# Optimization experiments

Measured on AMD Instinct MI355X. Metric: run time of the kernel, lower is better.

The kernel has to match this reference:

```python
import jax, jax.numpy as jnp
import numpy as np

EPS = 1e-5
K = 7        # deformable/spatial kernel size
GRID = 4     # local pool grid size


def conv(x, w, pad=0):
    # x: NCHW, w: OIHW
    return jax.lax.conv_general_dilated(
        x, w, (1, 1), [(pad, pad), (pad, pad)],
        dimension_numbers=('NCHW', 'OIHW', 'NCHW'))


def bn(x, g, b, m, v):
    # eval-mode batchnorm with running stats
    scale = (g * jax.lax.rsqrt(v + EPS))[None, :, None, None]
    return (x - m[None, :, None, None]) * scale + b[None, :, None, None]


def grid_sample(feat, grid):
    # bilinear, padding_mode='zeros', align_corners=False
    # feat: [b,c,h,w], grid: [b,h,w,2] with (x,y) in [-1,1]
    b, c, h, w = feat.shape
    gx = (grid[..., 0] + 1.0) * (w * 0.5) - 0.5
    gy = (grid[..., 1] + 1.0) * (h * 0.5) - 0.5
    x0 = jnp.floor(gx)
    y0 = jnp.floor(gy)
    wx = gx - x0
    wy = gy - y0
    feat_flat = feat.reshape(b, c, h * w)

    def gather(yi, xi):
        valid = (xi >= 0) & (xi < w) & (yi >= 0) & (yi < h)
        xi_c = jnp.clip(xi, 0, w - 1).astype(jnp.int32)
        yi_c = jnp.clip(yi, 0, h - 1).astype(jnp.int32)
        idx = (yi_c * w + xi_c).reshape(b, 1, h * w)
        vals = jnp.take_along_axis(feat_flat, idx, axis=2).reshape(b, c, h, w)
        return vals * valid[:, None].astype(feat.dtype)

    out = (gather(y0, x0) * ((1 - wx) * (1 - wy))[:, None]
           + gather(y0, x0 + 1) * (wx * (1 - wy))[:, None]
           + gather(y0 + 1, x0) * ((1 - wx) * wy)[:, None]
           + gather(y0 + 1, x0 + 1) * (wx * wy)[:, None])
    return out


def cmife_forward(x, align_w, align_g, align_b, align_m, align_v,
                  mlp_w1, mlp_w2, loc_w1, loc_w2, fusion_w,
                  off_w1, off_g, off_bt, off_m, off_v, off_w2, off_b2,
                  attn_w):
    # ---- align: 1x1 conv + BN + SiLU ----
    x = conv(x, align_w)
    x = bn(x, align_g, align_b, align_m, align_v)
    x = x * jax.nn.sigmoid(x)  # SiLU
    b_, c_, h_, w_ = x.shape

    # ---- LocalGlobalChannelAttention ----
    def mlp(z):
        return conv(jax.nn.relu(conv(z, mlp_w1)), mlp_w2)

    g_avg = mlp(jnp.mean(x, (2, 3), keepdims=True))
    g_max = mlp(jnp.max(x, (2, 3), keepdims=True))
    global_attn = g_avg + g_max
    # adaptive avg pool to GRIDxGRID (h,w divisible by GRID)
    loc = x.reshape(b_, c_, GRID, h_ // GRID, GRID, w_ // GRID).mean((3, 5))
    local_attn = conv(jax.nn.relu(conv(loc, loc_w1)), loc_w2)
    local_attn = local_attn.mean((2, 3), keepdims=True)
    alpha = jax.nn.sigmoid(fusion_w)
    ca = jax.nn.sigmoid(alpha * global_attn + (1 - alpha) * local_attn)
    x = ca * x

    # ---- DeformableSpatialAttention ----
    avg_out = jnp.mean(x, 1, keepdims=True)
    max_out = jnp.max(x, 1, keepdims=True)
    sf = jnp.concatenate([avg_out, max_out], axis=1)  # [b,2,h,w]
    o = jax.nn.relu(bn(conv(sf, off_w1, pad=1), off_g, off_bt, off_m, off_v))
    o = conv(o, off_w2, pad=1) + off_b2[None, :, None, None]  # [b,2*K*K,h,w]
    off = o.reshape(b_, 2, K * K, h_, w_).mean(2)             # [b,2,h,w]
    off = jnp.tanh(off) * 0.5
    off = jnp.transpose(off, (0, 2, 3, 1))                    # [b,h,w,2]
    gy, gx = jnp.meshgrid(jnp.linspace(-1.0, 1.0, h_),
                          jnp.linspace(-1.0, 1.0, w_), indexing='ij')
    base = jnp.stack([gx, gy], axis=-1)[None]                 # [1,h,w,2]
    dgrid = jnp.clip(base + off, -1.0, 1.0)
    sampled = grid_sample(sf, dgrid)                          # [b,2,h,w]
    sa = jax.nn.sigmoid(conv(sampled, attn_w, pad=K // 2))    # [b,1,h,w]
    return sa * x


def setup_inputs() -> dict:
    key = jax.random.key(0)
    ks = jax.random.split(key, 24)
    B, CIN, COUT, H, W, MID = 8, 256, 256, 160, 160, 16
    f = jnp.float32
    inp = {
        'x': jax.random.normal(ks[0], (B, CIN, H, W), f),
        'align_w': jax.random.normal(ks[1], (COUT, CIN, 1, 1), f) * 0.05,
        'align_g': jax.random.uniform(ks[2], (COUT,), f, 0.5, 1.5),
        'align_b': jax.random.normal(ks[3], (COUT,), f) * 0.1,
        'align_m': jax.random.normal(ks[4], (COUT,), f) * 0.1,
        'align_v': jax.random.uniform(ks[5], (COUT,), f, 0.5, 1.5),
        'mlp_w1': jax.random.normal(ks[6], (MID, COUT, 1, 1), f) * 0.1,
        'mlp_w2': jax.random.normal(ks[7], (COUT, MID, 1, 1), f) * 0.1,
        'loc_w1': jax.random.normal(ks[8], (MID, COUT, 1, 1), f) * 0.1,
        'loc_w2': jax.random.normal(ks[9], (COUT, MID, 1, 1), f) * 0.1,
        'fusion_w': jnp.float32(0.5),
        'off_w1': jax.random.normal(ks[10], (16, 2, 3, 3), f) * 0.1,
        'off_g': jax.random.uniform(ks[11], (16,), f, 0.5, 1.5),
        'off_bt': jax.random.normal(ks[12], (16,), f) * 0.1,
        'off_m': jax.random.normal(ks[13], (16,), f) * 0.1,
        'off_v': jax.random.uniform(ks[14], (16,), f, 0.5, 1.5),
        'off_w2': jax.random.normal(ks[15], (2 * K * K, 16, 3, 3), f) * 0.01,
        'off_b2': jax.random.normal(ks[16], (2 * K * K,), f) * 0.01,
        'attn_w': jax.random.normal(ks[17], (1, 2, K, K), f) * 0.1,
    }
    return inp


def reference(x, align_w, align_g, align_b, align_m, align_v,
              mlp_w1, mlp_w2, loc_w1, loc_w2, fusion_w,
              off_w1, off_g, off_bt, off_m, off_v, off_w2, off_b2,
              attn_w):
    return cmife_forward(x, align_w, align_g, align_b, align_m, align_v,
                         mlp_w1, mlp_w2, loc_w1, loc_w2, fusion_w,
                         off_w1, off_g, off_bt, off_m, off_v, off_w2, off_b2,
                         attn_w)
```

## Files before the change

### kernel.cpp

```cpp
#include <hip/hip_runtime.h>
#include <hip/hip_bf16.h>

#define HH 160
#define WW 160
#define HW 25600
#define NC 256
#define NB 8

typedef short short8 __attribute__((ext_vector_type(8)));
typedef float f32x4 __attribute__((ext_vector_type(4)));

__device__ __forceinline__ unsigned short f2bf(float f) {
    unsigned u = __float_as_uint(f);
    u += 0x7fffu + ((u >> 16) & 1u);
    return (unsigned short)(u >> 16);
}
__device__ __forceinline__ float bf2f(unsigned short h) {
    return __uint_as_float(((unsigned)h) << 16);
}

__global__ void k0_fold(const float* __restrict__ aw, const float* __restrict__ ag,
                        const float* __restrict__ ab, const float* __restrict__ am,
                        const float* __restrict__ av,
                        unsigned short* __restrict__ wpkh, unsigned short* __restrict__ wpkl,
                        float* __restrict__ biasp) {
    int co = blockIdx.x, t = threadIdx.x;
    float sc = ag[co] * rsqrtf(av[co] + 1e-5f);
    float w = aw[co * 256 + t] * sc;
    unsigned short h = f2bf(w);
    int kk = t >> 5, kq = t & 31;
    wpkh[kk * 10240 + co * 40 + kq] = h;
    wpkl[kk * 10240 + co * 40 + kq] = f2bf(w - bf2f(h));
    if (t == 0) biasp[co] = ab[co] - am[co] * sc;
}

__global__ void k0b_fold2(const float* __restrict__ ow2, const float* __restrict__ ob2,
                          float* __restrict__ weff, float* __restrict__ beff) {
    int t = threadIdx.x;
    if (t < 288) {
        int g = t / 144, r = t - g * 144;
        float s = 0.f;
        for (int q = 0; q < 49; q++) s += ow2[(size_t)(g * 49 + q) * 144 + r];
        weff[t] = s * (1.f / 49.f);
    }
    if (t < 2) {
        float s = 0.f;
        for (int q = 0; q < 49; q++) s += ob2[t * 49 + q];
        beff[t] = s * (1.f / 49.f);
    }
}

__global__ __launch_bounds__(256, 2) void k1_gemm(
    const float* __restrict__ X, const unsigned short* __restrict__ Wph,
    const unsigned short* __restrict__ Wpl,
    const float* __restrict__ biasp, float* __restrict__ xal) {
    __shared__ __align__(16) unsigned short Ah[10240];
    __shared__ __align__(16) unsigned short Al[10240];
    __shared__ __align__(16) unsigned short Bh[5120];
    __shared__ __align__(16) unsigned short Bl[5120];

    int t = threadIdx.x;
    int n0 = blockIdx.x * 128;
    int b  = blockIdx.y;
    const float* Xb = X + (size_t)b * NC * HW;

    int lane = t & 63, wv = t >> 6;
    int lcol = lane & 15, lq = lane >> 4;

    f32x4 acc[4][8];
#pragma unroll
    for (int i = 0; i < 4; i++)
#pragma unroll
        for (int j = 0; j < 8; j++) { f32x4 z = {0.f, 0.f, 0.f, 0.f}; acc[i][j] = z; }

    int bn2 = t & 63;
    int bkq = t >> 6;

    float2 pf[8];

#pragma unroll
    for (int j2 = 0; j2 < 2; j2++) {
        int kq = bkq + 4 * j2;
        const float* src = Xb + (size_t)(kq * 4) * HW + n0 + bn2 * 2;
#pragma unroll
        for (int j = 0; j < 2; j++) {
            pf[j2 * 4 + 2 * j]     = *(const float2*)(src + (size_t)(2 * j) * HW);
            pf[j2 * 4 + 2 * j + 1] = *(const float2*)(src + (size_t)(2 * j + 1) * HW);
        }
    }
    {
        const char* gah = (const char*)Wph;
        const char* gal = (const char*)Wpl;
#pragma unroll
        for (int i = 0; i < 5; i++) {
            int off = wv * 1024 + i * 4096;
            __builtin_amdgcn_global_load_lds(
                (const __attribute__((address_space(1))) unsigned int*)(gah + off + lane * 16),
                (__attribute__((address_space(3))) unsigned int*)((char*)Ah + off),
                16, 0, 0);
            __builtin_amdgcn_global_load_lds(
                (const __attribute__((address_space(1))) unsigned int*)(gal + off + lane * 16),
                (__attribute__((address_space(3))) unsigned int*)((char*)Al + off),
                16, 0, 0);
        }
    }

    for (int kk = 0; kk < 8; kk++) {
#pragma unroll
        for (int j2 = 0; j2 < 2; j2++) {
            int kq = bkq + 4 * j2;
            unsigned h0[2], h1[2], l0[2], l1[2];
#pragma unroll
            for (int j = 0; j < 2; j++) {
                float2 v0 = pf[j2 * 4 + 2 * j];
                float2 v1 = pf[j2 * 4 + 2 * j + 1];
                unsigned short a = f2bf(v0.x), bq = f2bf(v1.x);
                unsigned short c = f2bf(v0.y), d = f2bf(v1.y);
                h0[j] = (unsigned)a | ((unsigned)bq << 16);
                h1[j] = (unsigned)c | ((unsigned)d << 16);
                unsigned short la = f2bf(v0.x - bf2f(a)), lb = f2bf(v1.x - bf2f(bq));
                unsigned short lc = f2bf(v0.y - bf2f(c)), ld = f2bf(v1.y - bf2f(d));
                l0[j] = (unsigned)la | ((unsigned)lb << 16);
                l1[j] = (unsigned)lc | ((unsigned)ld << 16);
            }
            *(uint2*)(&Bh[(bn2 * 2) * 40 + kq * 4])     = make_uint2(h0[0], h0[1]);
            *(uint2*)(&Bh[(bn2 * 2 + 1) * 40 + kq * 4]) = make_uint2(h1[0], h1[1]);
            *(uint2*)(&Bl[(bn2 * 2) * 40 + kq * 4])     = make_uint2(l0[0], l0[1]);
            *(uint2*)(&Bl[(bn2 * 2 + 1) * 40 + kq * 4]) = make_uint2(l1[0], l1[1]);
        }
        __syncthreads();

        short8 afh[4], afl[4];
#pragma unroll
        for (int mt = 0; mt < 4; mt++) {
            afh[mt] = *(const short8*)(&Ah[(wv * 64 + mt * 16 + lcol) * 40 + lq * 8]);
            afl[mt] = *(const short8*)(&Al[(wv * 64 + mt * 16 + lcol) * 40 + lq * 8]);
        }
        if (kk < 7) {
#pragma unroll
            for (int j2 = 0; j2 < 2; j2++) {
                int kq = bkq + 4 * j2;
                const float* src = Xb + (size_t)((kk + 1) * 32 + kq * 4) * HW + n0 + bn2 * 2;
#pragma unroll
                for (int j = 0; j < 2; j++) {
                    pf[j2 * 4 + 2 * j]     = *(const float2*)(src + (size_t)(2 * j) * HW);
                    pf[j2 * 4 + 2 * j + 1] = *(const float2*)(src + (size_t)(2 * j + 1) * HW);
                }
            }
        }
#pragma unroll
        for (int nt = 0; nt < 8; nt++) {
            short8 bh = *(const short8*)(&Bh[(nt * 16 + lcol) * 40 + lq * 8]);
            short8 bl = *(const short8*)(&Bl[(nt * 16 + lcol) * 40 + lq * 8]);
#pragma unroll
            for (int mt = 0; mt < 4; mt++) {
                acc[mt][nt] = __builtin_amdgcn_mfma_f32_16x16x32_bf16(
                    afh[mt], bh, acc[mt][nt], 0, 0, 0);
                acc[mt][nt] = __builtin_amdgcn_mfma_f32_16x16x32_bf16(
                    afh[mt], bl, acc[mt][nt], 0, 0, 0);
                acc[mt][nt] = __builtin_amdgcn_mfma_f32_16x16x32_bf16(
                    afl[mt], bh, acc[mt][nt], 0, 0, 0);
            }
        }
        asm volatile("s_barrier" ::: "memory");
        if (kk < 7) {
            const char* gah = (const char*)(Wph + (kk + 1) * 10240);
            const char* gal = (const char*)(Wpl + (kk + 1) * 10240);
#pragma unroll
            for (int i = 0; i < 5; i++) {
                int off = wv * 1024 + i * 4096;
                __builtin_amdgcn_global_load_lds(
                    (const __attribute__((address_space(1))) unsigned int*)(gah + off + lane * 16),
                    (__attribute__((address_space(3))) unsigned int*)((char*)Ah + off),
                    16, 0, 0);
                __builtin_amdgcn_global_load_lds(
                    (const __attribute__((address_space(1))) unsigned int*)(gal + off + lane * 16),
                    (__attribute__((address_space(3))) unsigned int*)((char*)Al + off),
                    16, 0, 0);
            }
        }
    }
#pragma unroll
    for (int mt = 0; mt < 4; mt++) {
#pragma unroll
        for (int r = 0; r < 4; r++) {
            int co = wv * 64 + mt * 16 + lq * 4 + r;
            float bias = biasp[co];
            size_t rowbase = ((size_t)b * NC + co) * HW + n0;
#pragma unroll
            for (int nt = 0; nt < 8; nt++) {
                int n = nt * 16 + lcol;
                float y = acc[mt][nt][r] + bias;
                float z = y / (1.f + __expf(-y));
                xal[rowbase + n] = z;
            }
        }
    }
}

__global__ void ka_stats(const float* __restrict__ xal,
                         float* __restrict__ cellsum, float* __restrict__ cellmax) {
    __shared__ float rs[4][256], rm[4][256];
    int blk = blockIdx.x;
    int bc = blk >> 2, ch = blk & 3;
    const float* base = xal + (size_t)bc * HW + ch * 6400;
    int t = threadIdx.x;
    float s0 = 0.f, s1 = 0.f, s2 = 0.f, s3 = 0.f;
    float m0 = -3.4e38f, m1 = -3.4e38f, m2 = -3.4e38f, m3 = -3.4e38f;
    int c = (t < 160) ? t : t - 160;
#pragma unroll 5
    for (int i = 0; i < 25; i++) {
        float v = base[i * 256 + t];
        bool w0 = c < 40;
        bool w1 = (c >= 40) & (c < 80);
        bool w2 = (c >= 80) & (c < 120);
        bool w3 = c >= 120;
        s0 += w0 ? v : 0.f;  m0 = w0 ? fmaxf(m0, v) : m0;
        s1 += w1 ? v : 0.f;  m1 = w1 ? fmaxf(m1, v) : m1;
        s2 += w2 ? v : 0.f;  m2 = w2 ? fmaxf(m2, v) : m2;
        s3 += w3 ? v : 0.f;  m3 = w3 ? fmaxf(m3, v) : m3;
        c += 96; if (c >= 160) c -= 160;
    }
    rs[0][t] = s0; rs[1][t] = s1; rs[2][t] = s2; rs[3][t] = s3;
    rm[0][t] = m0; rm[1][t] = m1; rm[2][t] = m2; rm[3][t] = m3;
    __syncthreads();
    int g = t >> 6, i0 = t & 63;
    float sv = rs[g][i0] + rs[g][i0 + 64] + rs[g][i0 + 128] + rs[g][i0 + 192];
    float mv = fmaxf(fmaxf(rm[g][i0], rm[g][i0 + 64]),
                     fmaxf(rm[g][i0 + 128], rm[g][i0 + 192]));
#pragma unroll
    for (int off = 32; off >= 1; off >>= 1) {
        sv += __shfl_down(sv, off, 64);
        mv = fmaxf(mv, __shfl_down(mv, off, 64));
    }
    if (i0 == 0) {
        cellsum[bc * 16 + ch * 4 + g] = sv;
        cellmax[bc * 16 + ch * 4 + g] = mv;
    }
}

__global__ void kb_attn(const float* __restrict__ cellsum, const float* __restrict__ cellmax,
                        const float* __restrict__ mw1, const float* __restrict__ mw2,
                        const float* __restrict__ lw1, const float* __restrict__ lw2,
                        const float* __restrict__ fw, float* __restrict__ ca) {
    __shared__ float avgS[256], maxS[256], locS[256 * 16], hid[32], hlS[256];
    int b = blockIdx.x, t = threadIdx.x;
    float s = 0.f, m = -3.4e38f;
#pragma unroll
    for (int cell = 0; cell < 16; cell++) {
        float cs = cellsum[(b * 256 + t) * 16 + cell];
        float cm = cellmax[(b * 256 + t) * 16 + cell];
        s += cs;
        m = fmaxf(m, cm);
        locS[t * 16 + cell] = cs * (1.f / 1600.f);
    }
    avgS[t] = s * (1.f / 25600.f);
    maxS[t] = m;
    __syncthreads();
    if (t < 32) {
        int j = t & 15;
        const float* w1 = mw1 + j * 256;
        const float* src = (t < 16) ? avgS : maxS;
        float h = 0.f;
        for (int c = 0; c < 256; c++) h += w1[c] * src[c];
        hid[t] = fmaxf(h, 0.f);
    }
    {
        int cell = t >> 4, j = t & 15;
        const float* w1 = lw1 + j * 256;
        float h = 0.f;
        for (int c = 0; c < 256; c++) h += w1[c] * locS[c * 16 + cell];
        hlS[t] = fmaxf(h, 0.f);
    }
    __syncthreads();
    float ga = 0.f, gm = 0.f;
#pragma unroll
    for (int j = 0; j < 16; j++) {
        float w2 = mw2[t * 16 + j];
        ga += w2 * hid[j];
        gm += w2 * hid[16 + j];
    }
    float la = 0.f;
#pragma unroll
    for (int cell = 0; cell < 16; cell++)
#pragma unroll
        for (int j = 0; j < 16; j++)
            la += lw2[t * 16 + j] * hlS[cell * 16 + j];
    float alpha = 1.f / (1.f + expf(-fw[0]));
    float pre = alpha * (ga + gm) + (1.f - alpha) * (la * (1.f / 16.f));
    ca[b * 256 + t] = 1.f / (1.f + expf(-pre));
}

__global__ void k3_sf(const float* __restrict__ xal,
                      const float* __restrict__ ca, float* __restrict__ sf) {
    __shared__ float cas[256];
    int b = blockIdx.y, t = threadIdx.x;
    cas[t] = ca[b * 256 + t];
    __syncthreads();
    int p = blockIdx.x * 256 + t;
    const float* base = xal + (size_t)b * NC * HW + p;
    float s0 = 0.f, m0 = -3.4e38f;
    for (int c = 0; c < 256; c++) {
        float a0 = cas[c] * base[(size_t)c * HW];
        s0 += a0;
        m0 = fmaxf(m0, a0);
    }
    sf[(size_t)b * 2 * HW + p]      = s0 * (1.f / 256.f);
    sf[(size_t)b * 2 * HW + HW + p] = m0;
}

__global__ void k4_conv1(const float* __restrict__ sf, const float* __restrict__ ow1,
                         const float* __restrict__ og, const float* __restrict__ obt,
                         const float* __restrict__ om, const float* __restrict__ ov,
                         float* __restrict__ o1) {
    __shared__ float wS[288], scS[16], shS[16];
    int b = blockIdx.y, t = threadIdx.x;
    for (int i = t; i < 288; i += 256) wS[i] = ow1[i];
    if (t < 16) {
        float sc = og[t] * rsqrtf(ov[t] + 1e-5f);
        scS[t] = sc;
        shS[t] = obt[t] - om[t] * sc;
    }
    __syncthreads();
    int p = blockIdx.x * 256 + t;
    int h = p / 160, w = p - h * 160;
    const float* a0 = sf + (size_t)b * 2 * HW;
    const float* a1 = a0 + HW;
    float in0[9], in1[9];
#pragma unroll
    for (int kh = 0; kh < 3; kh++)
#pragma unroll
        for (int kw = 0; kw < 3; kw++) {
            int hh = h + kh - 1, ww = w + kw - 1;
            bool ok = (hh >= 0) & (hh < 160) & (ww >= 0) & (ww < 160);
            int q = hh * 160 + ww;
            in0[kh * 3 + kw] = ok ? a0[q] : 0.f;
            in1[kh * 3 + kw] = ok ? a1[q] : 0.f;
        }
    float* outb = o1 + (size_t)b * 16 * HW + p;
#pragma unroll
    for (int j = 0; j < 16; j++) {
        float acc = 0.f;
#pragma unroll
        for (int k = 0; k < 9; k++)
            acc += wS[j * 18 + k] * in0[k] + wS[j * 18 + 9 + k] * in1[k];
        outb[(size_t)j * HW] = fmaxf(acc * scS[j] + shS[j], 0.f);
    }
}

__global__ void k5_sample(const float* __restrict__ o1, const float* __restrict__ weff,
                          const float* __restrict__ beff, const float* __restrict__ sf,
                          float* __restrict__ sampled) {
    __shared__ float tileS[16 * 18 * 18];
    __shared__ float wS[288];
    __shared__ float bS[2];
    int b = blockIdx.y, t = threadIdx.x;
    int ty0 = (blockIdx.x / 10) * 16, tx0 = (blockIdx.x % 10) * 16;
    const float* ob = o1 + (size_t)b * 16 * HW;
    for (int i = t; i < 288; i += 256) wS[i] = weff[i];
    if (t < 2) bS[t] = beff[t];
    for (int i = t; i < 16 * 18 * 18; i += 256) {
        int ci = i / 324, rem = i - ci * 324;
        int r = rem / 18, c = rem - r * 18;
        int gr = ty0 + r - 1, gc = tx0 + c - 1;
        bool ok = (gr >= 0) & (gr < 160) & (gc >= 0) & (gc < 160);
        tileS[i] = ok ? ob[(size_t)ci * HW + gr * 160 + gc] : 0.f;
    }
    __syncthreads();
    int ty = t >> 4, tx = t & 15;
    int h = ty0 + ty, w = tx0 + tx;
    int p = h * 160 + w;
    float s0 = bS[0], s1 = bS[1];
#pragma unroll
    for (int ci = 0; ci < 16; ci++) {
        const float* tb = &tileS[ci * 324 + ty * 18 + tx];
        const float* w0 = &wS[ci * 9];
        const float* w1 = &wS[144 + ci * 9];
#pragma unroll
        for (int kh = 0; kh < 3; kh++)
#pragma unroll
            for (int kw = 0; kw < 3; kw++) {
                float v = tb[kh * 18 + kw];
                s0 += w0[kh * 3 + kw] * v;
                s1 += w1[kh * 3 + kw] * v;
            }
    }
    float ox = tanhf(s0) * 0.5f;
    float oy = tanhf(s1) * 0.5f;
    float bx = w * (2.f / 159.f) - 1.f, by = h * (2.f / 159.f) - 1.f;
    float gxn = fminf(fmaxf(bx + ox, -1.f), 1.f);
    float gyn = fminf(fmaxf(by + oy, -1.f), 1.f);
    float gx = (gxn + 1.f) * 80.f - 0.5f;
    float gy = (gyn + 1.f) * 80.f - 0.5f;
    float x0f = floorf(gx), y0f = floorf(gy);
    float wx = gx - x0f, wy = gy - y0f;
    int ix0 = (int)x0f, iy0 = (int)y0f;
    const float* f0 = sf + (size_t)b * 2 * HW;
    const float* f1 = f0 + HW;
    float r0 = 0.f, r1 = 0.f;
#pragma unroll
    for (int dy = 0; dy < 2; dy++)
#pragma unroll
        for (int dx = 0; dx < 2; dx++) {
            int xi = ix0 + dx, yi = iy0 + dy;
            float wgt = (dx ? wx : 1.f - wx) * (dy ? wy : 1.f - wy);
            if ((xi >= 0) & (xi < 160) & (yi >= 0) & (yi < 160)) {
                int q = yi * 160 + xi;
                r0 += wgt * f0[q];
                r1 += wgt * f1[q];
            }
        }
    float* sb = sampled + (size_t)b * 2 * HW + p;
    sb[0] = r0;
    sb[HW] = r1;
}

__global__ void k5b_sa(const float* __restrict__ sampled, const float* __restrict__ attn_w,
                       float* __restrict__ sa) {
    __shared__ float wS[98];
    int b = blockIdx.y, t = threadIdx.x;
    if (t < 98) wS[t] = attn_w[t];
    __syncthreads();
    int p = blockIdx.x * 256 + t;
    int h = p / 160, w = p - h * 160;
    const float* s0 = sampled + (size_t)b * 2 * HW;
    const float* s1 = s0 + HW;
    float acc = 0.f;
#pragma unroll
    for (int kh = 0; kh < 7; kh++) {
        int hh = h + kh - 3;
        if (hh < 0 || hh >= 160) continue;
#pragma unroll
        for (int kw = 0; kw < 7; kw++) {
            int ww = w + kw - 3;
            if (ww < 0 || ww >= 160) continue;
            int q = hh * 160 + ww;
            acc += wS[kh * 7 + kw] * s0[q] + wS[49 + kh * 7 + kw] * s1[q];
        }
    }
    sa[(size_t)b * HW + p] = 1.f / (1.f + expf(-acc));
}

__global__ void k6_out(float* __restrict__ out, const float* __restrict__ ca,
                       const float* __restrict__ sa) {
    unsigned e4 = blockIdx.x * 256 + threadIdx.x;
    unsigned e = e4 * 4;
    unsigned b = e / (256u * HW);
    unsigned rem = e - b * (256u * HW);
    unsigned c = rem / HW;
    unsigned p = rem - c * HW;
    f32x4 v = *(f32x4*)(out + e);
    f32x4 s = *(const f32x4*)(sa + (size_t)b * HW + p);
    float cav = ca[b * 256 + c];
#pragma unroll
    for (int i = 0; i < 4; i++) v[i] = cav * s[i] * v[i];
    *(f32x4*)(out + e) = v;
}

extern "C" void kernel_launch(void* const* d_in, const int* in_sizes, int n_in,
                              void* d_out, int out_size, void* d_ws, size_t ws_size,
                              hipStream_t stream) {
    const float* x       = (const float*)d_in[0];
    const float* align_w = (const float*)d_in[1];
    const float* align_g = (const float*)d_in[2];
    const float* align_b = (const float*)d_in[3];
    const float* align_m = (const float*)d_in[4];
    const float* align_v = (const float*)d_in[5];
    const float* mlp_w1  = (const float*)d_in[6];
    const float* mlp_w2  = (const float*)d_in[7];
    const float* loc_w1  = (const float*)d_in[8];
    const float* loc_w2  = (const float*)d_in[9];
    const float* fusion  = (const float*)d_in[10];
    const float* off_w1  = (const float*)d_in[11];
    const float* off_g   = (const float*)d_in[12];
    const float* off_bt  = (const float*)d_in[13];
    const float* off_m   = (const float*)d_in[14];
    const float* off_v   = (const float*)d_in[15];
    const float* off_w2  = (const float*)d_in[16];
    const float* off_b2  = (const float*)d_in[17];
    const float* attn_w  = (const float*)d_in[18];
    float* out = (float*)d_out;

    char* wsb = (char*)d_ws;
    size_t off = 0;
    auto alloc = [&](size_t bytes) -> void* {
        off = (off + 255) & ~(size_t)255;
        void* p = wsb + off;
        off += bytes;
        return p;
    };
    float* xal = out;
    unsigned short* wph = (unsigned short*)alloc(81920 * 2);
    unsigned short* wpl = (unsigned short*)alloc(81920 * 2);
    float* biasp   = (float*)alloc(256 * 4);
    float* cellsum = (float*)alloc(32768 * 4);
    float* cellmax = (float*)alloc(32768 * 4);
    float* ca      = (float*)alloc(2048 * 4);
    float* sf      = (float*)alloc((size_t)NB * 2 * HW * 4);
    float* o1      = (float*)alloc((size_t)NB * 16 * HW * 4);
    float* sampled = (float*)alloc((size_t)NB * 2 * HW * 4);
    float* sa      = (float*)alloc((size_t)NB * HW * 4);
    float* weff    = (float*)alloc(288 * 4);
    float* beff    = (float*)alloc(2 * 4);
    (void)ws_size; (void)in_sizes; (void)n_in; (void)out_size;

    k0_fold<<<dim3(256), 256, 0, stream>>>(align_w, align_g, align_b, align_m, align_v,
                                           wph, wpl, biasp);
    k0b_fold2<<<dim3(1), 320, 0, stream>>>(off_w2, off_b2, weff, beff);
    k1_gemm<<<dim3(200, 8), 256, 0, stream>>>(x, wph, wpl, biasp, xal);
    ka_stats<<<dim3(8192), 256, 0, stream>>>(xal, cellsum, cellmax);
    kb_attn<<<dim3(8), 256, 0, stream>>>(cellsum, cellmax, mlp_w1, mlp_w2,
                                         loc_w1, loc_w2, fusion, ca);
    k3_sf<<<dim3(100, 8), 256, 0, stream>>>(xal, ca, sf);
    k4_conv1<<<dim3(100, 8), 256, 0, stream>>>(sf, off_w1, off_g, off_bt, off_m, off_v, o1);
    k5_sample<<<dim3(100, 8), 256, 0, stream>>>(o1, weff, beff, sf, sampled);
    k5b_sa<<<dim3(100, 8), 256, 0, stream>>>(sampled, attn_w, sa);
    k6_out<<<dim3(51200), 256, 0, stream>>>(out, ca, sa);
}
```

Baseline: 682.0 us.

## Use 512-thread GEMM blocks and vectorize per-cell stats reduction

The align GEMM now runs 8 waves per block instead of 4, so each wave owns 32 output channels instead of 64. The B-tile staging is reorganized so each thread loads 8 scalar rows of one column and writes a single 16-byte LDS store. This halves per-wave accumulator registers and aims for more waves in flight, at the cost of more barrier participants and smaller per-wave MFMA reuse. Separately, the stats kernel uses 320 threads with float4 loads mapped directly to grid cells, replacing the predicated four-way accumulation with a simpler reduction.

```diff
diff --git a/kernel.cpp b/kernel.cpp
--- a/kernel.cpp
+++ b/kernel.cpp
@@ -50,7 +50,7 @@
     }
 }
 
-__global__ __launch_bounds__(256, 2) void k1_gemm(
+__global__ __launch_bounds__(512, 4) void k1_gemm(
     const float* __restrict__ X, const unsigned short* __restrict__ Wph,
     const unsigned short* __restrict__ Wpl,
     const float* __restrict__ biasp, float* __restrict__ xal) {
@@ -67,108 +67,29 @@
     int lane = t & 63, wv = t >> 6;
     int lcol = lane & 15, lq = lane >> 4;
 
-    f32x4 acc[4][8];
-#pragma unroll
-    for (int i = 0; i < 4; i++)
+    f32x4 acc[2][8];
+#pragma unroll
+    for (int i = 0; i < 2; i++)
 #pragma unroll
         for (int j = 0; j < 8; j++) { f32x4 z = {0.f, 0.f, 0.f, 0.f}; acc[i][j] = z; }
 
-    int bn2 = t & 63;
-    int bkq = t >> 6;
-
-    float2 pf[8];
-
-#pragma unroll
-    for (int j2 = 0; j2 < 2; j2++) {
-        int kq = bkq + 4 * j2;
-        const float* src = Xb + (size_t)(kq * 4) * HW + n0 + bn2 * 2;
-#pragma unroll
-        for (int j = 0; j < 2; j++) {
-            pf[j2 * 4 + 2 * j]     = *(const float2*)(src + (size_t)(2 * j) * HW);
-            pf[j2 * 4 + 2 * j + 1] = *(const float2*)(src + (size_t)(2 * j + 1) * HW);
-        }
+    int bn  = t & 127;
+    int kq2 = t >> 7;
+
+    float pf[8];
+
+    {
+        const float* src = Xb + (size_t)(kq2 * 8) * HW + n0 + bn;
+#pragma unroll
+        for (int j = 0; j < 8; j++) pf[j] = src[(size_t)j * HW];
     }
     {
         const char* gah = (const char*)Wph;
         const char* gal = (const char*)Wpl;
 #pragma unroll
-        for (int i = 0; i < 5; i++) {
-            int off = wv * 1024 + i * 4096;
-            __builtin_amdgcn_global_load_lds(
-                (const __attribute__((address_space(1))) unsigned int*)(gah + off + lane * 16),
-                (__attribute__((address_space(3))) unsigned int*)((char*)Ah + off),
-                16, 0, 0);
-            __builtin_amdgcn_global_load_lds(
-                (const __attribute__((address_space(1))) unsigned int*)(gal + off + lane * 16),
-                (__attribute__((address_space(3))) unsigned int*)((char*)Al + off),
-                16, 0, 0);
-        }
-    }
-
-    for (int kk = 0; kk < 8; kk++) {
-#pragma unroll
-        for (int j2 = 0; j2 < 2; j2++) {
-            int kq = bkq + 4 * j2;
-            unsigned h0[2], h1[2], l0[2], l1[2];
-#pragma unroll
-            for (int j = 0; j < 2; j++) {
-                float2 v0 = pf[j2 * 4 + 2 * j];
-                float2 v1 = pf[j2 * 4 + 2 * j + 1];
-                unsigned short a = f2bf(v0.x), bq = f2bf(v1.x);
-                unsigned short c = f2bf(v0.y), d = f2bf(v1.y);
-                h0[j] = (unsigned)a | ((unsigned)bq << 16);
-                h1[j] = (unsigned)c | ((unsigned)d << 16);
-                unsigned short la = f2bf(v0.x - bf2f(a)), lb = f2bf(v1.x - bf2f(bq));
-                unsigned short lc = f2bf(v0.y - bf2f(c)), ld = f2bf(v1.y - bf2f(d));
-                l0[j] = (unsigned)la | ((unsigned)lb << 16);
-                l1[j] = (unsigned)lc | ((unsigned)ld << 16);
-            }
-            *(uint2*)(&Bh[(bn2 * 2) * 40 + kq * 4])     = make_uint2(h0[0], h0[1]);
-            *(uint2*)(&Bh[(bn2 * 2 + 1) * 40 + kq * 4]) = make_uint2(h1[0], h1[1]);
-            *(uint2*)(&Bl[(bn2 * 2) * 40 + kq * 4])     = make_uint2(l0[0], l0[1]);
-            *(uint2*)(&Bl[(bn2 * 2 + 1) * 40 + kq * 4]) = make_uint2(l1[0], l1[1]);
-        }
-        __syncthreads();
-
-        short8 afh[4], afl[4];
-#pragma unroll
-        for (int mt = 0; mt < 4; mt++) {
-            afh[mt] = *(const short8*)(&Ah[(wv * 64 + mt * 16 + lcol) * 40 + lq * 8]);
-            afl[mt] = *(const short8*)(&Al[(wv * 64 + mt * 16 + lcol) * 40 + lq * 8]);
-        }
-        if (kk < 7) {
-#pragma unroll
-            for (int j2 = 0; j2 < 2; j2++) {
-                int kq = bkq + 4 * j2;
-                const float* src = Xb + (size_t)((kk + 1) * 32 + kq * 4) * HW + n0 + bn2 * 2;
-#pragma unroll
-                for (int j = 0; j < 2; j++) {
-                    pf[j2 * 4 + 2 * j]     = *(const float2*)(src + (size_t)(2 * j) * HW);
-                    pf[j2 * 4 + 2 * j + 1] = *(const float2*)(src + (size_t)(2 * j + 1) * HW);
-                }
-            }
-        }
-#pragma unroll
-        for (int nt = 0; nt < 8; nt++) {
-            short8 bh = *(const short8*)(&Bh[(nt * 16 + lcol) * 40 + lq * 8]);
-            short8 bl = *(const short8*)(&Bl[(nt * 16 + lcol) * 40 + lq * 8]);
-#pragma unroll
-            for (int mt = 0; mt < 4; mt++) {
-                acc[mt][nt] = __builtin_amdgcn_mfma_f32_16x16x32_bf16(
-                    afh[mt], bh, acc[mt][nt], 0, 0, 0);
-                acc[mt][nt] = __builtin_amdgcn_mfma_f32_16x16x32_bf16(
-                    afh[mt], bl, acc[mt][nt], 0, 0, 0);
-                acc[mt][nt] = __builtin_amdgcn_mfma_f32_16x16x32_bf16(
-                    afl[mt], bh, acc[mt][nt], 0, 0, 0);
-            }
-        }
-        asm volatile("s_barrier" ::: "memory");
-        if (kk < 7) {
-            const char* gah = (const char*)(Wph + (kk + 1) * 10240);
-            const char* gal = (const char*)(Wpl + (kk + 1) * 10240);
-#pragma unroll
-            for (int i = 0; i < 5; i++) {
-                int off = wv * 1024 + i * 4096;
+        for (int i = 0; i < 3; i++) {
+            if (i < 2 || wv < 4) {
+                int off = i * 8192 + wv * 1024;
                 __builtin_amdgcn_global_load_lds(
                     (const __attribute__((address_space(1))) unsigned int*)(gah + off + lane * 16),
                     (__attribute__((address_space(3))) unsigned int*)((char*)Ah + off),
@@ -180,11 +101,74 @@
             }
         }
     }
-#pragma unroll
-    for (int mt = 0; mt < 4; mt++) {
+
+    for (int kk = 0; kk < 8; kk++) {
+        {
+            unsigned hi[4], lo[4];
+#pragma unroll
+            for (int j = 0; j < 4; j++) {
+                unsigned short a = f2bf(pf[2 * j]);
+                unsigned short c = f2bf(pf[2 * j + 1]);
+                hi[j] = (unsigned)a | ((unsigned)c << 16);
+                unsigned short la = f2bf(pf[2 * j] - bf2f(a));
+                unsigned short lc = f2bf(pf[2 * j + 1] - bf2f(c));
+                lo[j] = (unsigned)la | ((unsigned)lc << 16);
+            }
+            *(uint4*)(&Bh[bn * 40 + kq2 * 8]) = make_uint4(hi[0], hi[1], hi[2], hi[3]);
+            *(uint4*)(&Bl[bn * 40 + kq2 * 8]) = make_uint4(lo[0], lo[1], lo[2], lo[3]);
+        }
+        __syncthreads();
+
+        short8 afh[2], afl[2];
+#pragma unroll
+        for (int mt = 0; mt < 2; mt++) {
+            afh[mt] = *(const short8*)(&Ah[(wv * 32 + mt * 16 + lcol) * 40 + lq * 8]);
+            afl[mt] = *(const short8*)(&Al[(wv * 32 + mt * 16 + lcol) * 40 + lq * 8]);
+        }
+        if (kk < 7) {
+            const float* src = Xb + (size_t)((kk + 1) * 32 + kq2 * 8) * HW + n0 + bn;
+#pragma unroll
+            for (int j = 0; j < 8; j++) pf[j] = src[(size_t)j * HW];
+        }
+#pragma unroll
+        for (int nt = 0; nt < 8; nt++) {
+            short8 bh = *(const short8*)(&Bh[(nt * 16 + lcol) * 40 + lq * 8]);
+            short8 bl = *(const short8*)(&Bl[(nt * 16 + lcol) * 40 + lq * 8]);
+#pragma unroll
+            for (int mt = 0; mt < 2; mt++) {
+                acc[mt][nt] = __builtin_amdgcn_mfma_f32_16x16x32_bf16(
+                    afh[mt], bh, acc[mt][nt], 0, 0, 0);
+                acc[mt][nt] = __builtin_amdgcn_mfma_f32_16x16x32_bf16(
+                    afh[mt], bl, acc[mt][nt], 0, 0, 0);
+                acc[mt][nt] = __builtin_amdgcn_mfma_f32_16x16x32_bf16(
+                    afl[mt], bh, acc[mt][nt], 0, 0, 0);
+            }
+        }
+        asm volatile("s_barrier" ::: "memory");
+        if (kk < 7) {
+            const char* gah = (const char*)(Wph + (kk + 1) * 10240);
+            const char* gal = (const char*)(Wpl + (kk + 1) * 10240);
+#pragma unroll
+            for (int i = 0; i < 3; i++) {
+                if (i < 2 || wv < 4) {
+                    int off = i * 8192 + wv * 1024;
+                    __builtin_amdgcn_global_load_lds(
+                        (const __attribute__((address_space(1))) unsigned int*)(gah + off + lane * 16),
+                        (__attribute__((address_space(3))) unsigned int*)((char*)Ah + off),
+                        16, 0, 0);
+                    __builtin_amdgcn_global_load_lds(
+                        (const __attribute__((address_space(1))) unsigned int*)(gal + off + lane * 16),
+                        (__attribute__((address_space(3))) unsigned int*)((char*)Al + off),
+                        16, 0, 0);
+                }
+            }
+        }
+    }
+#pragma unroll
+    for (int mt = 0; mt < 2; mt++) {
 #pragma unroll
         for (int r = 0; r < 4; r++) {
-            int co = wv * 64 + mt * 16 + lq * 4 + r;
+            int co = wv * 32 + mt * 16 + lq * 4 + r;
             float bias = biasp[co];
             size_t rowbase = ((size_t)b * NC + co) * HW + n0;
 #pragma unroll
@@ -200,42 +184,39 @@
 
 __global__ void ka_stats(const float* __restrict__ xal,
                          float* __restrict__ cellsum, float* __restrict__ cellmax) {
-    __shared__ float rs[4][256], rm[4][256];
+    __shared__ float rs[320], rm[320];
     int blk = blockIdx.x;
-    int bc = blk >> 2, ch = blk & 3;
-    const float* base = xal + (size_t)bc * HW + ch * 6400;
+    int bc = blk >> 2, band = blk & 3;
+    const float* base = xal + (size_t)bc * HW + band * 6400;
     int t = threadIdx.x;
-    float s0 = 0.f, s1 = 0.f, s2 = 0.f, s3 = 0.f;
-    float m0 = -3.4e38f, m1 = -3.4e38f, m2 = -3.4e38f, m3 = -3.4e38f;
-    int c = (t < 160) ? t : t - 160;
-#pragma unroll 5
-    for (int i = 0; i < 25; i++) {
-        float v = base[i * 256 + t];
-        bool w0 = c < 40;
-        bool w1 = (c >= 40) & (c < 80);
-        bool w2 = (c >= 80) & (c < 120);
-        bool w3 = c >= 120;
-        s0 += w0 ? v : 0.f;  m0 = w0 ? fmaxf(m0, v) : m0;
-        s1 += w1 ? v : 0.f;  m1 = w1 ? fmaxf(m1, v) : m1;
-        s2 += w2 ? v : 0.f;  m2 = w2 ? fmaxf(m2, v) : m2;
-        s3 += w3 ? v : 0.f;  m3 = w3 ? fmaxf(m3, v) : m3;
-        c += 96; if (c >= 160) c -= 160;
-    }
-    rs[0][t] = s0; rs[1][t] = s1; rs[2][t] = s2; rs[3][t] = s3;
-    rm[0][t] = m0; rm[1][t] = m1; rm[2][t] = m2; rm[3][t] = m3;
-    __syncthreads();
-    int g = t >> 6, i0 = t & 63;
-    float sv = rs[g][i0] + rs[g][i0 + 64] + rs[g][i0 + 128] + rs[g][i0 + 192];
-    float mv = fmaxf(fmaxf(rm[g][i0], rm[g][i0 + 64]),
-                     fmaxf(rm[g][i0 + 128], rm[g][i0 + 192]));
-#pragma unroll
-    for (int off = 32; off >= 1; off >>= 1) {
-        sv += __shfl_down(sv, off, 64);
-        mv = fmaxf(mv, __shfl_down(mv, off, 64));
-    }
-    if (i0 == 0) {
-        cellsum[bc * 16 + ch * 4 + g] = sv;
-        cellmax[bc * 16 + ch * 4 + g] = mv;
+    int col = (t % 40) / 10;
+    float s = 0.f, m = -3.4e38f;
+#pragma unroll
+    for (int i = 0; i < 5; i++) {
+        f32x4 v = *(const f32x4*)(base + (size_t)(i * 320 + t) * 4);
+        s += (v[0] + v[1]) + (v[2] + v[3]);
+        m = fmaxf(fmaxf(fmaxf(m, v[0]), fmaxf(v[1], v[2])), v[3]);
+    }
+    int slot = (t / 40) * 10 + (t % 10);
+    rs[col * 80 + slot] = s;
+    rm[col * 80 + slot] = m;
+    __syncthreads();
+    if (t < 64) {
+#pragma unroll
+        for (int c2 = 0; c2 < 4; c2++) {
+            float sv = rs[c2 * 80 + t] + ((t < 16) ? rs[c2 * 80 + 64 + t] : 0.f);
+            float mv = fmaxf(rm[c2 * 80 + t],
+                             (t < 16) ? rm[c2 * 80 + 64 + t] : -3.4e38f);
+#pragma unroll
+            for (int off = 32; off >= 1; off >>= 1) {
+                sv += __shfl_down(sv, off, 64);
+                mv = fmaxf(mv, __shfl_down(mv, off, 64));
+            }
+            if (t == 0) {
+                cellsum[bc * 16 + band * 4 + c2] = sv;
+                cellmax[bc * 16 + band * 4 + c2] = mv;
+            }
+        }
     }
 }
 
@@ -507,8 +488,8 @@
     k0_fold<<<dim3(256), 256, 0, stream>>>(align_w, align_g, align_b, align_m, align_v,
                                            wph, wpl, biasp);
     k0b_fold2<<<dim3(1), 320, 0, stream>>>(off_w2, off_b2, weff, beff);
-    k1_gemm<<<dim3(200, 8), 256, 0, stream>>>(x, wph, wpl, biasp, xal);
-    ka_stats<<<dim3(8192), 256, 0, stream>>>(xal, cellsum, cellmax);
+    k1_gemm<<<dim3(200, 8), 512, 0, stream>>>(x, wph, wpl, biasp, xal);
+    ka_stats<<<dim3(8192), 320, 0, stream>>>(xal, cellsum, cellmax);
     kb_attn<<<dim3(8), 256, 0, stream>>>(cellsum, cellmax, mlp_w1, mlp_w2,
                                          loc_w1, loc_w2, fusion, ca);
     k3_sf<<<dim3(100, 8), 256, 0, stream>>>(xal, ca, sf);
```

Measured after the change: 708.6 us. +3.9%, slower.
